# Kernel optimization log

Hardware: AMD Instinct MI355X
Metric: run time of the kernel (lower is better)

## Reference

```python
import jax, jax.numpy as jnp
import numpy as np
from jax import lax

H = 1024
W = 1024
WIN = 32
STR = 16
NH = (H - WIN) // STR + 1  # 63
N = NH * NH                # 3969 patches
DN3 = ('NCDHW', 'OIDHW', 'NCDHW')
DN2 = ('NCHW', 'OIHW', 'NCHW')


def setup_inputs() -> dict:
    key = jax.random.key(0)
    ks = jax.random.split(key, 13)
    r = lambda k, s, sc=0.05: jax.random.normal(k, s, dtype=jnp.float32) * sc
    return {
        'x1': jax.random.normal(ks[0], (1, 1, 1, H, W), jnp.float32),
        'x2': jax.random.normal(ks[1], (1, 1, 1, H, W), jnp.float32),
        'conv1_w': r(ks[2], (24, 1, 2, 8, 8)),      # Conv3d(1,24,(2,8,8)) [O,I,D,H,W]
        'conv1_b': r(ks[3], (24,)),
        'conv2_w': r(ks[4], (60, 24, 5, 5)),         # Conv2d(24,60,5)
        'conv2_b': r(ks[5], (60,)),
        'deconv2_w': r(ks[6], (60, 24, 5, 5)),       # ConvTranspose2d(60,24,5) [I,O,kH,kW]
        'deconv2_b': r(ks[7], (24,)),
        'deconv1_w': r(ks[8], (24, 1, 2, 8, 8)),     # ConvTranspose3d(24,1,(2,8,8)) [I,O,D,H,W]
        'deconv1_b': r(ks[9], (1,)),
        'lin_w': r(ks[10], (N, 2), 0.5),             # per-patch Linear(2,1) weights
        'lin_b': r(ks[11], (N,), 0.5),               # per-patch Linear(2,1) bias
        'linear1_w': r(ks[12], (1, 1), 0.5),         # Linear(1,1,bias=False)
    }


def _conv(x, w, b, dn):
    nd = w.ndim - 2
    y = lax.conv_general_dilated(x, w, (1,) * nd, 'VALID', dimension_numbers=dn)
    return y + b.reshape((1, -1) + (1,) * nd)


def _convT(x, w, b, dn):
    # stride-1, pad-0 transposed conv == full-pad conv with flipped, IO-swapped kernel
    nd = w.ndim - 2
    wf = jnp.flip(w, axis=tuple(range(2, w.ndim))).swapaxes(0, 1)  # [O,I,*k]
    pad = [(k - 1, k - 1) for k in w.shape[2:]]
    y = lax.conv_general_dilated(x, wf, (1,) * nd, pad, dimension_numbers=dn)
    return y + b.reshape((1, -1) + (1,) * nd)


def reference(x1, x2, conv1_w, conv1_b, conv2_w, conv2_b, deconv2_w, deconv2_b,
              deconv1_w, deconv1_b, lin_w, lin_b, linear1_w):
    x = jnp.concatenate([x1, x2], axis=2)[0, 0]  # [2,H,W]
    idx = (jnp.arange(NH) * STR)[:, None] + jnp.arange(WIN)[None, :]  # [NH,32]
    # unfold dims 3,4 with window 32 / stride 16 -> [2,NH,NW,32,32]
    patches = x[:, idx[:, None, :, None], idx[None, :, None, :]]
    outX = patches.reshape(2, N, WIN, WIN).transpose(1, 0, 2, 3)[:, None]  # [N,1,2,32,32]
    h = jax.nn.elu(_conv(outX, conv1_w, conv1_b, DN3))        # [N,24,1,25,25]
    h = jax.nn.relu(_conv(h[:, :, 0], conv2_w, conv2_b, DN2))  # [N,60,21,21]
    h = jax.nn.elu(_convT(h, deconv2_w, deconv2_b, DN2))       # [N,24,25,25]
    h = _convT(h[:, :, None], deconv1_w, deconv1_b, DN3)       # [N,1,2,32,32]
    # per-patch Linear(2,1) over depth channels, batched over all patches
    p = jnp.einsum('nchw,nc->nhw', h[:, 0], lin_w) + lin_b[:, None, None]  # [N,32,32]
    p = p.reshape(NH, NH, WIN, WIN)
    # col2im: overlap-add fold, block 32, stride 16 -> [H,W]
    recon = jnp.zeros((H, W), jnp.float32).at[idx[:, None, :, None], idx[None, :, None, :]].add(p)
    outX2 = recon * linear1_w[0, 0]  # Linear(1,1,bias=False) per pixel
    return x2 - outX2.reshape(x2.shape)
```

## Files before the change

kernel.cpp:

```cpp
#include <hip/hip_runtime.h>
#include <hip/hip_bf16.h>

static constexpr int H_ = 1024;
static constexpr int W_ = 1024;
static constexpr int STR_ = 16;
static constexpr int NH_ = 63;
static constexpr int NPATCH_ = NH_ * NH_;
static constexpr int NGRP_ = 32;
static constexpr int NBLK_ = NH_ * NGRP_;

typedef short bf16x8 __attribute__((ext_vector_type(8)));
typedef short short4v __attribute__((ext_vector_type(4)));
typedef float f32x4 __attribute__((ext_vector_type(4)));

static constexpr int GAP16   = 49200;
static constexpr int CP0     = 49216;
static constexpr int CP1     = 55360;
static constexpr int SH2_0   = 49216;
static constexpr int SH2SZ   = 52920;
static constexpr int SH2_1   = SH2_0 + SH2SZ;
static constexpr int ZROW    = 155056;
static constexpr int H3SZ    = 30000;
static constexpr int SWC0    = 60000;
static constexpr int SWC1    = 64096;
static constexpr int SPA     = 68192;
static constexpr int LDS_BYTES = 155200;

__device__ __forceinline__ unsigned short f2bf(float x) {
    __hip_bfloat16 b = __float2bfloat16(x);
    return __builtin_bit_cast(unsigned short, b);
}

__device__ __forceinline__ f32x4 mfma_bf16(bf16x8 a, bf16x8 b, f32x4 c) {
    return __builtin_amdgcn_mfma_f32_16x16x32_bf16(a, b, c, 0, 0, 0);
}

__device__ __forceinline__ float elu_neg(float x) { return __expf(x) - 1.f; }

__global__ __launch_bounds__(1024, 4) void fused_patch_kernel(
    const float* __restrict__ x1, const float* __restrict__ x2,
    const float* __restrict__ c1b, const float* __restrict__ c2b,
    const float* __restrict__ d2b, const float* __restrict__ d1b,
    const float* __restrict__ lin_w, const float* __restrict__ lin_b,
    const unsigned short* __restrict__ w1frag,
    const unsigned short* __restrict__ w2frag,
    const unsigned short* __restrict__ dw2frag,
    const float* __restrict__ dw1,
    float* __restrict__ recon)
{
    __shared__ alignas(16) char sbuf[LDS_BYTES];
    const int b   = blockIdx.x;
    const int pi  = b / NGRP_, g = b - pi * NGRP_;
    const int pj0 = 2 * g;
    const int npat = (pj0 + 1 < NH_) ? 2 : 1;
    const int n0  = pi * NH_ + pj0;
    const int n1  = (npat == 2) ? (n0 + 1) : n0;
    const int Y0  = pi * STR_, X0 = pj0 * STR_;
    const int t   = (int)threadIdx.x;
    const int wv  = t >> 6, lane = t & 63;
    const int ln15 = lane & 15, quad = lane >> 4;

    bf16x8 w1b[8];
    #pragma unroll
    for (int gg = 0; gg < 8; ++gg)
        w1b[gg] = *(const bf16x8*)(w1frag + (gg * 64 + lane) * 8);
    const float lw00 = lin_w[2 * n0], lw01 = lin_w[2 * n0 + 1];
    const float lw10 = lin_w[2 * n1], lw11 = lin_w[2 * n1 + 1];
    const float lbn0 = lin_b[n0], lbn1 = lin_b[n1];
    const float d1b0 = d1b[0];
    const float c1b0 = c1b[ln15];
    const float c1b1 = (16 + ln15 < 24) ? c1b[16 + ln15] : 0.f;
    float c2bias[4];
    #pragma unroll
    for (int nt = 0; nt < 4; ++nt) {
        int o = nt * 16 + ln15;
        c2bias[nt] = (o < 60) ? c2b[o] : 0.f;
    }
    const float db0 = d2b[ln15];
    const float db1 = (16 + ln15 < 24) ? d2b[16 + ln15] : 0.f;
    float dwp[4] = {0.f, 0.f, 0.f, 0.f};
    {
        int r0 = t >> 5, c0 = t & 31;
        if (c0 < 24) {
            dwp[0] = dw1[(c0 * 2 + 0) * 64 + r0];
            dwp[1] = dw1[(c0 * 2 + 1) * 64 + r0];
        }
        int k1 = t + 1024, r1 = k1 >> 5, c1 = k1 & 31;
        if (c1 < 24) {
            dwp[2] = dw1[(c1 * 2 + 0) * 64 + r1];
            dwp[3] = dw1[(c1 * 2 + 1) * 64 + r1];
        }
    }

    if (t < 4)       ((float*)(sbuf + GAP16))[t] = 0.f;
    else if (t < 8)  ((float*)(sbuf + SH2_1))[t - 4] = 0.f;
    else if (t < 42) ((float*)(sbuf + ZROW))[t - 8] = 0.f;
    #pragma unroll
    for (int it = 0; it < 3; ++it) {
        int k = t + it * 1024;
        int d = (k >= 1536) ? 1 : 0;
        int rem = k - d * 1536;
        int y = rem / 48, x = rem - y * 48;
        int xg = X0 + x; if (xg > W_ - 1) xg = W_ - 1;
        unsigned short bb = f2bf((d ? x2 : x1)[(Y0 + y) * W_ + xg]);
        int row = (d * 32 + y) * 48;
        ((unsigned short*)(sbuf + CP0))[row + x] = bb;
        if (x > 0) ((unsigned short*)(sbuf + CP1))[row + x - 1] = bb;
    }
    __syncthreads();

    for (int tl = wv; tl < 65; tl += 16) {
        int m = tl * 16 + ln15; if (m > 1024) m = 1024;
        int u = m / 41, v = m - u * 41;
        const char* cps = sbuf + ((v & 1) ? CP1 : CP0);
        const int vb2 = (v & ~1) * 2;
        f32x4 acc[2];
        acc[0] = (f32x4){0.f, 0.f, 0.f, 0.f};
        acc[1] = (f32x4){0.f, 0.f, 0.f, 0.f};
        #pragma unroll
        for (int kc = 0; kc < 4; ++kc) {
            const int idx8 = kc * 4 + quad;
            const int dd = idx8 >> 3, pp = idx8 & 7;
            const unsigned int* ap = (const unsigned int*)(cps + (dd * 32 + u + pp) * 96 + vb2);
            union { unsigned int u4[4]; bf16x8 v8; } af;
            af.u4[0] = ap[0]; af.u4[1] = ap[1]; af.u4[2] = ap[2]; af.u4[3] = ap[3];
            acc[0] = mfma_bf16(af.v8, w1b[kc * 2 + 0], acc[0]);
            acc[1] = mfma_bf16(af.v8, w1b[kc * 2 + 1], acc[1]);
        }
        #pragma unroll
        for (int ntp = 0; ntp < 2; ++ntp) {
            const int c = ntp * 16 + ln15;
            if (c < 24) {
                const float bias = ntp ? c1b1 : c1b0;
                #pragma unroll
                for (int r = 0; r < 4; ++r) {
                    int mm = tl * 16 + quad * 4 + r;
                    if (mm < 1025) {
                        float hv = acc[ntp][r] + bias;
                        hv = hv > 0.f ? hv : elu_neg(hv);
                        *(unsigned short*)(sbuf + mm * 48 + c * 2) = f2bf(hv);
                    }
                }
            }
        }
    }
    __syncthreads();

    auto s2pass = [&](int t0, int t1) {
        const bool h1 = (t1 < 56);
        int ab[2], loc[2], Pp[2];
        #pragma unroll
        for (int i = 0; i < 2; ++i) {
            int tt = i ? (h1 ? t1 : t0) : t0;
            int P = (tt >= 28) ? 1 : 0;
            int lc = tt - P * 28;
            int mm = lc * 16 + ln15; if (mm > 440) mm = 440;
            int y = mm / 21, x = mm - y * 21;
            ab[i] = (y * 41 + P * 16 + x) * 48;
            loc[i] = lc; Pp[i] = P;
        }
        f32x4 acc2[2][4];
        #pragma unroll
        for (int i = 0; i < 2; ++i)
            #pragma unroll
            for (int nt = 0; nt < 4; ++nt)
                acc2[i][nt] = (f32x4){0.f, 0.f, 0.f, 0.f};
        const unsigned short* wb = w2frag + lane * 8;
        #pragma unroll
        for (int p = 0; p < 5; ++p) {
            #pragma unroll
            for (int q = 0; q < 5; ++q) {
                const int tap  = p * 5 + q;
                const int toff = (p * 41 + q) * 48;
                bf16x8 bfr[4];
                #pragma unroll
                for (int nt = 0; nt < 4; ++nt)
                    bfr[nt] = *(const bf16x8*)(wb + (tap * 4 + nt) * 512);
                {
                    bf16x8 a = *(const bf16x8*)(sbuf + ab[0] + toff + quad * 16);
                    #pragma unroll
                    for (int nt = 0; nt < 4; ++nt)
                        acc2[0][nt] = mfma_bf16(a, bfr[nt], acc2[0][nt]);
                }
                if (h1) {
                    bf16x8 a = *(const bf16x8*)(sbuf + ab[1] + toff + quad * 16);
                    #pragma unroll
                    for (int nt = 0; nt < 4; ++nt)
                        acc2[1][nt] = mfma_bf16(a, bfr[nt], acc2[1][nt]);
                }
            }
        }
        #pragma unroll
        for (int i = 0; i < 2; ++i) {
            if (i == 1 && !h1) continue;
            unsigned short* base = (unsigned short*)(sbuf + SH2_0 + Pp[i] * SH2SZ);
            #pragma unroll
            for (int r = 0; r < 4; ++r) {
                int pix = loc[i] * 16 + quad * 4 + r;
                if (pix < 441) {
                    unsigned short* rowp = base + pix * 60;
                    #pragma unroll
                    for (int nt = 0; nt < 4; ++nt) {
                        int o = nt * 16 + ln15;
                        if (o < 60)
                            rowp[o] = f2bf(fmaxf(acc2[i][nt][r] + c2bias[nt], 0.f));
                    }
                }
            }
        }
    };
    s2pass(wv, wv + 16);
    s2pass(wv + 32, wv + 48);
    __syncthreads();

    f32x4 acc3[5][2];
    {
        #pragma unroll
        for (int i = 0; i < 5; ++i) {
            acc3[i][0] = (f32x4){0.f, 0.f, 0.f, 0.f};
            acc3[i][1] = (f32x4){0.f, 0.f, 0.f, 0.f};
        }
        int uarr[5], varr[5], aoff[5];
        bool mval[5];
        #pragma unroll
        for (int i = 0; i < 5; ++i) {
            int t5 = wv + 16 * i;
            int P = (t5 >= 40) ? 1 : 0;
            int lc = t5 - P * 40;
            int m = lc * 16 + ln15;
            mval[i] = (m < 625);
            int mc = mval[i] ? m : 0;
            uarr[i] = mc / 25; varr[i] = mc - uarr[i] * 25;
            aoff[i] = SH2_0 + P * SH2SZ + (uarr[i] * 21 + varr[i]) * 120;
        }
        const unsigned short* db = dw2frag + lane * 8;
        #pragma unroll
        for (int dy = 0; dy < 5; ++dy) {
            #pragma unroll
            for (int dx = 0; dx < 5; ++dx) {
                const int tap = dy * 5 + dx;
                const int t2o = (dy * 21 + dx) * 120;
                bf16x8 bc0 = *(const bf16x8*)(db + tap * 2048);
                bf16x8 bc1 = *(const bf16x8*)(db + tap * 2048 + 512);
                bf16x8 bc2 = *(const bf16x8*)(db + tap * 2048 + 1024);
                bf16x8 bc3 = *(const bf16x8*)(db + tap * 2048 + 1536);
                #pragma unroll
                for (int i = 0; i < 5; ++i) {
                    int yv = uarr[i] - dy, xv = varr[i] - dx;
                    bool ok = mval[i] && ((unsigned)yv < 21u) && ((unsigned)xv < 21u);
                    int ra = ok ? (aoff[i] - t2o) : ZROW;
                    const char* ap = sbuf + ra + quad * 16;
                    short4v lo0 = *(const short4v*)(ap);
                    short4v hi0 = *(const short4v*)(ap + 8);
                    bf16x8 a0 = __builtin_shufflevector(lo0, hi0, 0, 1, 2, 3, 4, 5, 6, 7);
                    acc3[i][0] = mfma_bf16(a0, bc0, acc3[i][0]);
                    acc3[i][1] = mfma_bf16(a0, bc1, acc3[i][1]);
                    short4v lo1 = *(const short4v*)(ap + 64);
                    short4v hi1 = *(const short4v*)(ap + 72);
                    bf16x8 a1 = __builtin_shufflevector(lo1, hi1, 0, 1, 2, 3, 4, 5, 6, 7);
                    acc3[i][0] = mfma_bf16(a1, bc2, acc3[i][0]);
                    acc3[i][1] = mfma_bf16(a1, bc3, acc3[i][1]);
                }
            }
        }
    }
    __syncthreads();

    float* sp = (float*)(sbuf + SPA);
    {
        const int c1ok = (16 + ln15 < 24);
        #pragma unroll
        for (int i = 0; i < 5; ++i) {
            int t5 = wv + 16 * i;
            int P = (t5 >= 40) ? 1 : 0;
            int lc = t5 - P * 40;
            #pragma unroll
            for (int r = 0; r < 4; ++r) {
                int pix = lc * 16 + quad * 4 + r;
                if (pix < 625) {
                    unsigned short* rowp = (unsigned short*)(sbuf + P * H3SZ + pix * 48);
                    float hv = acc3[i][0][r] + db0;
                    rowp[ln15] = f2bf(hv > 0.f ? hv : elu_neg(hv));
                    if (c1ok) {
                        float hw = acc3[i][1][r] + db1;
                        rowp[16 + ln15] = f2bf(hw > 0.f ? hw : elu_neg(hw));
                    }
                }
            }
        }
    }
    {
        int r0 = t >> 5, c0 = t & 31;
        ((unsigned short*)(sbuf + SWC0))[r0 * 32 + c0] = f2bf(lw00 * dwp[0] + lw01 * dwp[1]);
        ((unsigned short*)(sbuf + SWC1))[r0 * 32 + c0] = f2bf(lw10 * dwp[0] + lw11 * dwp[1]);
        int k1 = t + 1024, r1 = k1 >> 5, c1 = k1 & 31;
        ((unsigned short*)(sbuf + SWC0))[r1 * 32 + c1] = f2bf(lw00 * dwp[2] + lw01 * dwp[3]);
        ((unsigned short*)(sbuf + SWC1))[r1 * 32 + c1] = f2bf(lw10 * dwp[2] + lw11 * dwp[3]);
    }
    sp[t] = 0.f; sp[t + 1024] = 0.f;
    __syncthreads();

    {
        int ntoff[4];
        #pragma unroll
        for (int nt = 0; nt < 4; ++nt) {
            int rv = nt * 16 + ln15;
            ntoff[nt] = (rv >> 3) * 32 + (rv & 7);
        }
        #pragma unroll
        for (int i = 0; i < 5; ++i) {
            int t5 = wv + 16 * i;
            int P = (t5 >= 40) ? 1 : 0;
            int lc = t5 - P * 40;
            int m = lc * 16 + ln15; if (m > 624) m = 624;
            bf16x8 a = *(const bf16x8*)(sbuf + P * H3SZ + m * 48 + quad * 16);
            const char* swc = sbuf + (P ? SWC1 : SWC0);
            bf16x8 wbv[4];
            #pragma unroll
            for (int nt = 0; nt < 4; ++nt)
                wbv[nt] = *(const bf16x8*)(swc + (nt * 16 + ln15) * 64 + quad * 16);
            float* spP = sp + P * 1024;
            int uvb[4]; bool pok[4];
            #pragma unroll
            for (int r = 0; r < 4; ++r) {
                int pix = lc * 16 + quad * 4 + r;
                pok[r] = (pix < 625);
                int pc = pok[r] ? pix : 0;
                uvb[r] = (pc / 25) * 32 + (pc % 25);
            }
            #pragma unroll
            for (int nt = 0; nt < 4; ++nt) {
                f32x4 acc4 = (f32x4){0.f, 0.f, 0.f, 0.f};
                acc4 = mfma_bf16(a, wbv[nt], acc4);
                #pragma unroll
                for (int r = 0; r < 4; ++r) {
                    if (pok[r])
                        atomicAdd(&spP[uvb[r] + ntoff[nt]], acc4[r]);
                }
            }
        }
    }
    __syncthreads();

    {
        int yy = t >> 5, xx = t & 31;
        float ob0 = d1b0 * (lw00 + lw01) + lbn0;
        atomicAdd(&recon[(Y0 + yy) * W_ + X0 + xx], sp[t] + ob0);
        if (npat == 2) {
            float ob1 = d1b0 * (lw10 + lw11) + lbn1;
            atomicAdd(&recon[(Y0 + yy) * W_ + X0 + 16 + xx], sp[t + 1024] + ob1);
        }
    }
}

__global__ void prep_kernel(const float* __restrict__ c1w,
                            const float* __restrict__ c2w,
                            const float* __restrict__ d2w,
                            unsigned short* __restrict__ w1frag,
                            unsigned short* __restrict__ w2frag,
                            unsigned short* __restrict__ dw2frag)
{
    int i = blockIdx.x * blockDim.x + threadIdx.x;
    if (i < 51200) {
        int j = i & 7, lane = (i >> 3) & 63;
        int ln15 = lane & 15, quad = lane >> 4;
        if (i < 4096) {
            int g = i >> 9;
            int kc = g >> 1, nt = g & 1;
            int nn = nt * 16 + ln15, k = kc * 32 + quad * 8 + j;
            w1frag[i] = f2bf((nn < 24) ? c1w[nn * 128 + k] : 0.f);
        }
        {
            int nt = (i >> 9) & 3, tap = i >> 11;
            int o = nt * 16 + ln15, c = quad * 8 + j;
            float v = (o < 60 && c < 24) ? c2w[(o * 24 + c) * 25 + tap] : 0.f;
            w2frag[i] = f2bf(v);
        }
        {
            int nt = (i >> 9) & 1, kc = (i >> 10) & 1, tap = i >> 11;
            int k = kc * 32 + quad * 8 + j, c = nt * 16 + ln15;
            float v = (k < 60 && c < 24) ? d2w[(k * 24 + c) * 25 + tap] : 0.f;
            dw2frag[i] = f2bf(v);
        }
    }
}

__global__ void finalize_kernel(const float* __restrict__ x2,
                                const float* __restrict__ l1w,
                                float* __restrict__ out)
{
    int i = blockIdx.x * blockDim.x + threadIdx.x;
    if (i < H_ * W_) {
        float r = out[i];
        out[i] = x2[i] - r * l1w[0];
    }
}

extern "C" void kernel_launch(void* const* d_in, const int* in_sizes, int n_in,
                              void* d_out, int out_size, void* d_ws, size_t ws_size,
                              hipStream_t stream)
{
    const float* x1  = (const float*)d_in[0];
    const float* x2  = (const float*)d_in[1];
    const float* c1w = (const float*)d_in[2];
    const float* c1b = (const float*)d_in[3];
    const float* c2w = (const float*)d_in[4];
    const float* c2b = (const float*)d_in[5];
    const float* d2w = (const float*)d_in[6];
    const float* d2b = (const float*)d_in[7];
    const float* d1w = (const float*)d_in[8];
    const float* d1b = (const float*)d_in[9];
    const float* lw  = (const float*)d_in[10];
    const float* lb  = (const float*)d_in[11];
    const float* l1w = (const float*)d_in[12];

    float*          out     = (float*)d_out;
    unsigned short* w1frag  = (unsigned short*)d_ws;
    unsigned short* w2frag  = (unsigned short*)((char*)d_ws + 8192);
    unsigned short* dw2frag = (unsigned short*)((char*)d_ws + 110592);

    hipMemsetAsync(d_out, 0, (size_t)H_ * W_ * sizeof(float), stream);
    prep_kernel<<<100, 512, 0, stream>>>(c1w, c2w, d2w, w1frag, w2frag, dw2frag);
    fused_patch_kernel<<<NBLK_, 1024, 0, stream>>>(x1, x2, c1b, c2b, d2b, d1b,
                                                   lw, lb, w1frag, w2frag, dw2frag,
                                                   d1w, out);
    finalize_kernel<<<(H_ * W_ + 255) / 256, 256, 0, stream>>>(x2, l1w, out);
}
```

Baseline: 1.396 ms.

## Swap MFMA operand order so accumulators hold channels per lane for vectorized stores

Every MFMA call now takes the weight fragment as A and the activation as B, which transposes the accumulator layout. Each lane then holds four consecutive output channels of one pixel instead of one channel across four pixels. The epilogues of conv1, conv2 and deconv2 pack those four channels into a single 8-byte LDS store, replacing scalar 2-byte stores. Biases are loaded as float4 per quad, and the final scatter computes one pixel base per lane rather than four divisions per lane. The aim is fewer LDS store instructions and less index arithmetic, at the cost of different LDS bank-access patterns for the wider stores.

```diff
diff --git a/kernel.cpp b/kernel.cpp
--- a/kernel.cpp
+++ b/kernel.cpp
@@ -68,16 +68,12 @@
     const float lw10 = lin_w[2 * n1], lw11 = lin_w[2 * n1 + 1];
     const float lbn0 = lin_b[n0], lbn1 = lin_b[n1];
     const float d1b0 = d1b[0];
-    const float c1b0 = c1b[ln15];
-    const float c1b1 = (16 + ln15 < 24) ? c1b[16 + ln15] : 0.f;
-    float c2bias[4];
-    #pragma unroll
-    for (int nt = 0; nt < 4; ++nt) {
-        int o = nt * 16 + ln15;
-        c2bias[nt] = (o < 60) ? c2b[o] : 0.f;
-    }
-    const float db0 = d2b[ln15];
-    const float db1 = (16 + ln15 < 24) ? d2b[16 + ln15] : 0.f;
+    const f32x4 c1bq0 = *(const f32x4*)(c1b + quad * 4);
+    f32x4 c1bq1 = (f32x4){0.f, 0.f, 0.f, 0.f};
+    if (quad < 2) c1bq1 = *(const f32x4*)(c1b + 16 + quad * 4);
+    const f32x4 d2bq0 = *(const f32x4*)(d2b + quad * 4);
+    f32x4 d2bq1 = (f32x4){0.f, 0.f, 0.f, 0.f};
+    if (quad < 2) d2bq1 = *(const f32x4*)(d2b + 16 + quad * 4);
     float dwp[4] = {0.f, 0.f, 0.f, 0.f};
     {
         int r0 = t >> 5, c0 = t & 31;
@@ -110,7 +106,8 @@
     __syncthreads();
 
     for (int tl = wv; tl < 65; tl += 16) {
-        int m = tl * 16 + ln15; if (m > 1024) m = 1024;
+        const int rawm = tl * 16 + ln15;
+        int m = rawm; if (m > 1024) m = 1024;
         int u = m / 41, v = m - u * 41;
         const char* cps = sbuf + ((v & 1) ? CP1 : CP0);
         const int vb2 = (v & ~1) * 2;
@@ -124,23 +121,28 @@
             const unsigned int* ap = (const unsigned int*)(cps + (dd * 32 + u + pp) * 96 + vb2);
             union { unsigned int u4[4]; bf16x8 v8; } af;
             af.u4[0] = ap[0]; af.u4[1] = ap[1]; af.u4[2] = ap[2]; af.u4[3] = ap[3];
-            acc[0] = mfma_bf16(af.v8, w1b[kc * 2 + 0], acc[0]);
-            acc[1] = mfma_bf16(af.v8, w1b[kc * 2 + 1], acc[1]);
-        }
-        #pragma unroll
-        for (int ntp = 0; ntp < 2; ++ntp) {
-            const int c = ntp * 16 + ln15;
-            if (c < 24) {
-                const float bias = ntp ? c1b1 : c1b0;
+            acc[0] = mfma_bf16(w1b[kc * 2 + 0], af.v8, acc[0]);
+            acc[1] = mfma_bf16(w1b[kc * 2 + 1], af.v8, acc[1]);
+        }
+        if (rawm < 1025) {
+            char* rowp = sbuf + rawm * 48;
+            short4v p0;
+            #pragma unroll
+            for (int r = 0; r < 4; ++r) {
+                float hv = acc[0][r] + c1bq0[r];
+                hv = hv > 0.f ? hv : elu_neg(hv);
+                p0[r] = (short)f2bf(hv);
+            }
+            *(short4v*)(rowp + quad * 8) = p0;
+            if (quad < 2) {
+                short4v p1;
                 #pragma unroll
                 for (int r = 0; r < 4; ++r) {
-                    int mm = tl * 16 + quad * 4 + r;
-                    if (mm < 1025) {
-                        float hv = acc[ntp][r] + bias;
-                        hv = hv > 0.f ? hv : elu_neg(hv);
-                        *(unsigned short*)(sbuf + mm * 48 + c * 2) = f2bf(hv);
-                    }
-                }
+                    float hw = acc[1][r] + c1bq1[r];
+                    hw = hw > 0.f ? hw : elu_neg(hw);
+                    p1[r] = (short)f2bf(hw);
+                }
+                *(short4v*)(rowp + 32 + quad * 8) = p1;
             }
         }
     }
@@ -180,31 +182,31 @@
                     bf16x8 a = *(const bf16x8*)(sbuf + ab[0] + toff + quad * 16);
                     #pragma unroll
                     for (int nt = 0; nt < 4; ++nt)
-                        acc2[0][nt] = mfma_bf16(a, bfr[nt], acc2[0][nt]);
+                        acc2[0][nt] = mfma_bf16(bfr[nt], a, acc2[0][nt]);
                 }
                 if (h1) {
                     bf16x8 a = *(const bf16x8*)(sbuf + ab[1] + toff + quad * 16);
                     #pragma unroll
                     for (int nt = 0; nt < 4; ++nt)
-                        acc2[1][nt] = mfma_bf16(a, bfr[nt], acc2[1][nt]);
+                        acc2[1][nt] = mfma_bf16(bfr[nt], a, acc2[1][nt]);
                 }
             }
         }
         #pragma unroll
         for (int i = 0; i < 2; ++i) {
             if (i == 1 && !h1) continue;
-            unsigned short* base = (unsigned short*)(sbuf + SH2_0 + Pp[i] * SH2SZ);
-            #pragma unroll
-            for (int r = 0; r < 4; ++r) {
-                int pix = loc[i] * 16 + quad * 4 + r;
-                if (pix < 441) {
-                    unsigned short* rowp = base + pix * 60;
+            int rawpix = loc[i] * 16 + ln15;
+            if (rawpix < 441) {
+                char* rowp = sbuf + SH2_0 + Pp[i] * SH2SZ + rawpix * 120;
+                #pragma unroll
+                for (int nt = 0; nt < 4; ++nt) {
+                    if (nt == 3 && quad == 3) continue;
+                    const f32x4 bq = *(const f32x4*)(c2b + nt * 16 + quad * 4);
+                    short4v pk;
                     #pragma unroll
-                    for (int nt = 0; nt < 4; ++nt) {
-                        int o = nt * 16 + ln15;
-                        if (o < 60)
-                            rowp[o] = f2bf(fmaxf(acc2[i][nt][r] + c2bias[nt], 0.f));
-                    }
+                    for (int r = 0; r < 4; ++r)
+                        pk[r] = (short)f2bf(fmaxf(acc2[i][nt][r] + bq[r], 0.f));
+                    *(short4v*)(rowp + nt * 32 + quad * 8) = pk;
                 }
             }
         }
@@ -253,13 +255,13 @@
                     short4v lo0 = *(const short4v*)(ap);
                     short4v hi0 = *(const short4v*)(ap + 8);
                     bf16x8 a0 = __builtin_shufflevector(lo0, hi0, 0, 1, 2, 3, 4, 5, 6, 7);
-                    acc3[i][0] = mfma_bf16(a0, bc0, acc3[i][0]);
-                    acc3[i][1] = mfma_bf16(a0, bc1, acc3[i][1]);
+                    acc3[i][0] = mfma_bf16(bc0, a0, acc3[i][0]);
+                    acc3[i][1] = mfma_bf16(bc1, a0, acc3[i][1]);
                     short4v lo1 = *(const short4v*)(ap + 64);
                     short4v hi1 = *(const short4v*)(ap + 72);
                     bf16x8 a1 = __builtin_shufflevector(lo1, hi1, 0, 1, 2, 3, 4, 5, 6, 7);
-                    acc3[i][0] = mfma_bf16(a1, bc2, acc3[i][0]);
-                    acc3[i][1] = mfma_bf16(a1, bc3, acc3[i][1]);
+                    acc3[i][0] = mfma_bf16(bc2, a1, acc3[i][0]);
+                    acc3[i][1] = mfma_bf16(bc3, a1, acc3[i][1]);
                 }
             }
         }
@@ -268,23 +270,31 @@
 
     float* sp = (float*)(sbuf + SPA);
     {
-        const int c1ok = (16 + ln15 < 24);
         #pragma unroll
         for (int i = 0; i < 5; ++i) {
             int t5 = wv + 16 * i;
             int P = (t5 >= 40) ? 1 : 0;
             int lc = t5 - P * 40;
-            #pragma unroll
-            for (int r = 0; r < 4; ++r) {
-                int pix = lc * 16 + quad * 4 + r;
-                if (pix < 625) {
-                    unsigned short* rowp = (unsigned short*)(sbuf + P * H3SZ + pix * 48);
-                    float hv = acc3[i][0][r] + db0;
-                    rowp[ln15] = f2bf(hv > 0.f ? hv : elu_neg(hv));
-                    if (c1ok) {
-                        float hw = acc3[i][1][r] + db1;
-                        rowp[16 + ln15] = f2bf(hw > 0.f ? hw : elu_neg(hw));
+            int pix = lc * 16 + ln15;
+            if (pix < 625) {
+                char* rowp = sbuf + P * H3SZ + pix * 48;
+                short4v p0;
+                #pragma unroll
+                for (int r = 0; r < 4; ++r) {
+                    float hv = acc3[i][0][r] + d2bq0[r];
+                    hv = hv > 0.f ? hv : elu_neg(hv);
+                    p0[r] = (short)f2bf(hv);
+                }
+                *(short4v*)(rowp + quad * 8) = p0;
+                if (quad < 2) {
+                    short4v p1;
+                    #pragma unroll
+                    for (int r = 0; r < 4; ++r) {
+                        float hw = acc3[i][1][r] + d2bq1[r];
+                        hw = hw > 0.f ? hw : elu_neg(hw);
+                        p1[r] = (short)f2bf(hw);
                     }
+                    *(short4v*)(rowp + 32 + quad * 8) = p1;
                 }
             }
         }
@@ -301,41 +311,33 @@
     __syncthreads();
 
     {
-        int ntoff[4];
-        #pragma unroll
-        for (int nt = 0; nt < 4; ++nt) {
-            int rv = nt * 16 + ln15;
-            ntoff[nt] = (rv >> 3) * 32 + (rv & 7);
+        int qoff[4];
+        #pragma unroll
+        for (int r = 0; r < 4; ++r) {
+            int qr = quad * 4 + r;
+            qoff[r] = (qr >> 3) * 32 + (qr & 7);
         }
         #pragma unroll
         for (int i = 0; i < 5; ++i) {
             int t5 = wv + 16 * i;
             int P = (t5 >= 40) ? 1 : 0;
             int lc = t5 - P * 40;
-            int m = lc * 16 + ln15; if (m > 624) m = 624;
-            bf16x8 a = *(const bf16x8*)(sbuf + P * H3SZ + m * 48 + quad * 16);
+            int rawpix = lc * 16 + ln15;
+            bool pok = (rawpix < 625);
+            int pc = pok ? rawpix : 624;
+            bf16x8 a = *(const bf16x8*)(sbuf + P * H3SZ + pc * 48 + quad * 16);
             const char* swc = sbuf + (P ? SWC1 : SWC0);
-            bf16x8 wbv[4];
-            #pragma unroll
-            for (int nt = 0; nt < 4; ++nt)
-                wbv[nt] = *(const bf16x8*)(swc + (nt * 16 + ln15) * 64 + quad * 16);
             float* spP = sp + P * 1024;
-            int uvb[4]; bool pok[4];
-            #pragma unroll
-            for (int r = 0; r < 4; ++r) {
-                int pix = lc * 16 + quad * 4 + r;
-                pok[r] = (pix < 625);
-                int pc = pok[r] ? pix : 0;
-                uvb[r] = (pc / 25) * 32 + (pc % 25);
-            }
+            int uvbase = (pc / 25) * 32 + (pc % 25);
             #pragma unroll
             for (int nt = 0; nt < 4; ++nt) {
+                bf16x8 wbv = *(const bf16x8*)(swc + (nt * 16 + ln15) * 64 + quad * 16);
                 f32x4 acc4 = (f32x4){0.f, 0.f, 0.f, 0.f};
-                acc4 = mfma_bf16(a, wbv[nt], acc4);
-                #pragma unroll
-                for (int r = 0; r < 4; ++r) {
-                    if (pok[r])
-                        atomicAdd(&spP[uvb[r] + ntoff[nt]], acc4[r]);
+                acc4 = mfma_bf16(wbv, a, acc4);
+                if (pok) {
+                    #pragma unroll
+                    for (int r = 0; r < 4; ++r)
+                        atomicAdd(&spP[uvbase + nt * 64 + qoff[r]], acc4[r]);
                 }
             }
         }
```

New measurement: 1.345 ms. -3.7%, faster.
